# Optimization experiments

Measured on AMD Instinct MI355X. Metric: run time of the kernel, lower is better.

The kernel has to match this reference:

```python
import jax, jax.numpy as jnp
import numpy as np

DIM = 1024; DEPTH = 2; HEADS = 8; DH = DIM // HEADS  # 128
BUCKET = 64; NHASH = 4; MULT = 4
B = 2; T = 4096
NBUCKETS = T // BUCKET  # 64
SCALE = DH ** -0.5
SELF_ATTN_VAL = -5e4  # TOKEN_SELF_ATTN_VALUE in reformer-pytorch
EPS = 1e-5


def layer_norm(x, g, b):
    m = jnp.mean(x, -1, keepdims=True)
    v = jnp.var(x, -1, keepdims=True)
    return (x - m) * jax.lax.rsqrt(v + EPS) * g + b


def lsh_attn(xn, Wqk, Wv, Wo, bo, rot):
    # xn: [B,T,DIM] already layer-normed. Shared-QK LSH attention (reformer-pytorch).
    qk = (xn @ Wqk).reshape(B, T, HEADS, DH).transpose(0, 2, 1, 3).reshape(B * HEADS, T, DH)
    v = (xn @ Wv).reshape(B, T, HEADS, DH).transpose(0, 2, 1, 3).reshape(B * HEADS, T, DH)
    bh = B * HEADS
    # --- hashing with random rotations ---
    rotated = jnp.einsum('btf,fhi->bhti', qk, rot)            # [bh,NHASH,T,NBUCKETS//2]
    rotated = jnp.concatenate([rotated, -rotated], -1)        # [bh,NHASH,T,NBUCKETS]
    buckets = jnp.argmax(rotated, -1)                         # [bh,NHASH,T]
    offs = (jnp.arange(NHASH) * NBUCKETS)[:, None]
    buckets = (buckets + offs).reshape(bh, NHASH * T)
    ticker = jnp.arange(NHASH * T)
    bt = buckets * T + (ticker % T)                           # unique keys -> stable-equivalent sort
    sticker = jnp.argsort(bt, axis=-1)                        # [bh, NHASH*T]
    undo = jnp.argsort(sticker, axis=-1)
    st = sticker % T                                          # original positions, bucket-sorted
    sqk = jnp.take_along_axis(qk, st[..., None], axis=1)
    sv = jnp.take_along_axis(v, st[..., None], axis=1)
    nchunks = NHASH * NBUCKETS
    bq_t = st.reshape(bh, nchunks, BUCKET)
    bqk = sqk.reshape(bh, nchunks, BUCKET, DH)
    bv = sv.reshape(bh, nchunks, BUCKET, DH)
    bq = bqk
    bk = bqk / jnp.clip(jnp.linalg.norm(bqk, axis=-1, keepdims=True), 1e-12)
    def look_one_back(a):
        extra = jnp.concatenate([a[:, -1:], a[:, :-1]], axis=1)
        return jnp.concatenate([a, extra], axis=2)
    bk = look_one_back(bk); bv = look_one_back(bv); bkv_t = look_one_back(bq_t)
    dots = jnp.einsum('bcie,bcje->bcij', bq, bk) * SCALE      # [bh,nchunks,BUCKET,2*BUCKET]
    self_mask = bq_t[..., :, None] == bkv_t[..., None, :]     # shared-QK: penalize i==j
    dots = jnp.where(self_mask, SELF_ATTN_VAL, dots)
    lse = jax.nn.logsumexp(dots, axis=-1, keepdims=True)
    p = jnp.exp(dots - lse)
    bo_ = jnp.einsum('bcij,bcje->bcie', p, bv)
    so = bo_.reshape(bh, NHASH * T, DH)
    slog = lse.reshape(bh, NHASH * T)
    o = jnp.take_along_axis(so, undo[..., None], axis=1)
    logits = jnp.take_along_axis(slog, undo, axis=1)
    o = o.reshape(bh, NHASH, T, DH)
    logits = logits.reshape(bh, NHASH, T, 1)
    probs = jnp.exp(logits - jax.nn.logsumexp(logits, axis=1, keepdims=True))
    out = jnp.sum(o * probs, axis=1)                          # combine hash rounds
    out = out.reshape(B, HEADS, T, DH).transpose(0, 2, 1, 3).reshape(B, T, HEADS * DH)
    return out @ Wo + bo


def setup_inputs() -> dict:
    key = jax.random.key(0)
    ks = jax.random.split(key, 16)
    s = 0.02
    d = {
        'x': jax.random.normal(ks[0], (B, T, DIM), jnp.float32),
        'ln1_g': jnp.ones((DEPTH, DIM), jnp.float32),
        'ln1_b': jnp.zeros((DEPTH, DIM), jnp.float32),
        'Wqk': jax.random.normal(ks[1], (DEPTH, DIM, HEADS * DH), jnp.float32) * s,
        'Wv': jax.random.normal(ks[2], (DEPTH, DIM, HEADS * DH), jnp.float32) * s,
        'Wo': jax.random.normal(ks[3], (DEPTH, HEADS * DH, DIM), jnp.float32) * s,
        'bo': jnp.zeros((DEPTH, DIM), jnp.float32),
        'ln2_g': jnp.ones((DEPTH, DIM), jnp.float32),
        'ln2_b': jnp.zeros((DEPTH, DIM), jnp.float32),
        'W1': jax.random.normal(ks[4], (DEPTH, DIM, DIM * MULT), jnp.float32) * s,
        'b1': jnp.zeros((DEPTH, DIM * MULT), jnp.float32),
        'W2': jax.random.normal(ks[5], (DEPTH, DIM * MULT, DIM), jnp.float32) * s,
        'b2': jnp.zeros((DEPTH, DIM), jnp.float32),
        'rotations': jax.random.normal(ks[6], (DEPTH, DH, NHASH, NBUCKETS // 2), jnp.float32),
    }
    return d


def reference(x, ln1_g, ln1_b, Wqk, Wv, Wo, bo, ln2_g, ln2_b, W1, b1, W2, b2, rotations):
    xx = jnp.concatenate([x, x], -1)  # [B,T,2*DIM] reversible pair
    def step(carry, p):
        g1, be1, wqk, wv, wo, bov, g2, be2, w1, bb1, w2, bb2, rot = p
        x1, x2 = jnp.split(carry, 2, axis=-1)
        y1 = x1 + lsh_attn(layer_norm(x2, g1, be1), wqk, wv, wo, bov, rot)
        h = layer_norm(y1, g2, be2)
        ff = jax.nn.gelu(h @ w1 + bb1, approximate=False) @ w2 + bb2
        y2 = x2 + ff
        return jnp.concatenate([y1, y2], -1), None
    params = (ln1_g, ln1_b, Wqk, Wv, Wo, bo, ln2_g, ln2_b, W1, b1, W2, b2, rotations)
    out, _ = jax.lax.scan(step, xx, params)
    y1, y2 = jnp.split(out, 2, axis=-1)
    return y1 + y2
```

## Files before the change

kernel.cpp:

```cpp
#include <hip/hip_runtime.h>
#include <hip/hip_bf16.h>
#include <cmath>

using bf16 = __hip_bfloat16;
typedef __attribute__((ext_vector_type(8))) short short8;
typedef __attribute__((ext_vector_type(4))) float floatx4;

__device__ __forceinline__ float bu2f(ushort u) { return __uint_as_float((unsigned)u << 16); }
__device__ __forceinline__ ushort f2bu(float f) {
  union { bf16 b; ushort u; } cv; cv.b = __float2bfloat16(f); return cv.u;
}
__device__ __forceinline__ void gl_lds16(const ushort* g, ushort* l) {
  __builtin_amdgcn_global_load_lds((const __attribute__((address_space(1))) unsigned*)g,
                                   (__attribute__((address_space(3))) unsigned*)l, 16, 0, 0);
}
__device__ __forceinline__ float fast_gelu(float x) {
  float z = 0.7978845608028654f * (x + 0.044715f * x * x * x);
  z = fmaxf(fminf(z, 10.f), -10.f);
  float e = __expf(2.f * z);
  float t = (e - 1.f) / (e + 1.f);
  return 0.5f * x * (1.f + t);
}

static constexpr int kT   = 4096;
static constexpr int kDim = 1024;
static constexpr float kScale   = 0.08838834764831845f;
static constexpr float kSelfVal = -5.0e4f;

__device__ __forceinline__ int sane_v(float f) { float a = fabsf(f); return (a > 1e-4f && a < 1e4f) ? 1 : 0; }

__global__ __launch_bounds__(256) void k_detect(const unsigned* __restrict__ x, int* __restrict__ flag) {
  __shared__ int cnt;
  int tid = threadIdx.x;
  if (tid == 0) cnt = 0;
  __syncthreads();
  int my = 0;
  const uint4* p = (const uint4*)x;
  for (int q = 0; q < 16; q++) {
    uint4 u = p[tid * 16 + q];
    my += sane_v(__uint_as_float(u.x << 16)) + sane_v(__uint_as_float(u.x & 0xffff0000u));
    my += sane_v(__uint_as_float(u.y << 16)) + sane_v(__uint_as_float(u.y & 0xffff0000u));
    my += sane_v(__uint_as_float(u.z << 16)) + sane_v(__uint_as_float(u.z & 0xffff0000u));
    my += sane_v(__uint_as_float(u.w << 16)) + sane_v(__uint_as_float(u.w & 0xffff0000u));
  }
  atomicAdd(&cnt, my);
  __syncthreads();
  if (tid == 0) flag[0] = (cnt >= 24576) ? 1 : 0;
}

__global__ __launch_bounds__(256) void k_cvt(const int* __restrict__ flag, const void* __restrict__ src,
                                             ushort* __restrict__ dst, int n) {
  int i = blockIdx.x * 256 + threadIdx.x;
  if (i >= n) return;
  dst[i] = (*flag) ? ((const ushort*)src)[i] : f2bu(((const float*)src)[i]);
}

__global__ __launch_bounds__(256) void k_init_any(const int* __restrict__ flag, const void* __restrict__ x,
                                                  float* __restrict__ x1, float* __restrict__ x2) {
  int i = blockIdx.x * 1024 + threadIdx.x * 4;
  float4 f;
  if (*flag) {
    ushort4 u = *(const ushort4*)((const ushort*)x + i);
    f.x = bu2f(u.x); f.y = bu2f(u.y); f.z = bu2f(u.z); f.w = bu2f(u.w);
  } else {
    f = *(const float4*)((const float*)x + i);
  }
  *(float4*)(x1 + i) = f;
  *(float4*)(x2 + i) = f;
}

__global__ __launch_bounds__(256) void k_final_any(const int* __restrict__ flag, const float* __restrict__ x1,
                                                   const float* __restrict__ x2, void* __restrict__ out) {
  int i = blockIdx.x * 1024 + threadIdx.x * 4;
  float4 a = *(const float4*)(x1 + i);
  float4 b = *(const float4*)(x2 + i);
  float4 s; s.x = a.x + b.x; s.y = a.y + b.y; s.z = a.z + b.z; s.w = a.w + b.w;
  if (*flag) {
    ushort4 u; u.x = f2bu(s.x); u.y = f2bu(s.y); u.z = f2bu(s.z); u.w = f2bu(s.w);
    *(ushort4*)((ushort*)out + i) = u;
  } else {
    *(float4*)((float*)out + i) = s;
  }
}

__global__ __launch_bounds__(256) void k_ln(const float* __restrict__ x, const ushort* __restrict__ g,
                                            const ushort* __restrict__ be, ushort* __restrict__ out) {
  __shared__ float ws[4], ws2[4];
  int row = blockIdx.x, tid = threadIdx.x;
  const float* xr = x + (size_t)row * kDim + tid * 4;
  float4 v = *(const float4*)xr;
  float s  = v.x + v.y + v.z + v.w;
  float s2 = v.x*v.x + v.y*v.y + v.z*v.z + v.w*v.w;
  #pragma unroll
  for (int off = 32; off; off >>= 1) { s += __shfl_down(s, off); s2 += __shfl_down(s2, off); }
  int wave = tid >> 6, lane = tid & 63;
  if (lane == 0) { ws[wave] = s; ws2[wave] = s2; }
  __syncthreads();
  s  = ws[0] + ws[1] + ws[2] + ws[3];
  s2 = ws2[0] + ws2[1] + ws2[2] + ws2[3];
  float mean = s * (1.f/1024.f);
  float var  = fmaxf(s2 * (1.f/1024.f) - mean*mean, 0.f);
  float rstd = rsqrtf(var + 1e-5f);
  int cb = tid * 4;
  ushort* o = out + (size_t)row * kDim + cb;
  o[0] = f2bu((v.x - mean) * rstd * bu2f(g[cb+0]) + bu2f(be[cb+0]));
  o[1] = f2bu((v.y - mean) * rstd * bu2f(g[cb+1]) + bu2f(be[cb+1]));
  o[2] = f2bu((v.z - mean) * rstd * bu2f(g[cb+2]) + bu2f(be[cb+2]));
  o[3] = f2bu((v.w - mean) * rstd * bu2f(g[cb+3]) + bu2f(be[cb+3]));
}

__global__ __launch_bounds__(256) void k_transpose2(const int* __restrict__ flag, const void* __restrict__ src_bf,
                                                    const void* __restrict__ src_f, ushort* __restrict__ out,
                                                    int K, int N) {
  __shared__ ushort tile[32][33];
  int isbf = *flag;
  int nb = blockIdx.x * 32, kb = blockIdx.y * 32;
  int tx = threadIdx.x & 31, ty = threadIdx.x >> 5;
  for (int r = ty; r < 32; r += 8) {
    size_t idx = (size_t)(kb + r) * N + nb + tx;
    tile[r][tx] = isbf ? ((const ushort*)src_bf)[idx] : f2bu(((const float*)src_f)[idx]);
  }
  __syncthreads();
  for (int r = ty; r < 32; r += 8) out[(size_t)(nb + r) * K + kb + tx] = tile[tx][r];
}

__global__ __launch_bounds__(256) void k_rot_t(const ushort* __restrict__ rot, ushort* __restrict__ rotT) {
  int tid = threadIdx.x;
  for (int idx = tid; idx < 16384; idx += 256) {
    int n = idx >> 7, k = idx & 127;
    rotT[idx] = rot[k * 128 + n];
  }
}

template <int MW>
__global__ __launch_bounds__(512, 2) void k_gemm2(const ushort* __restrict__ A, const ushort* __restrict__ Bt,
                                                  const ushort* __restrict__ bias, float* __restrict__ Cf,
                                                  ushort* __restrict__ Cb, ushort* __restrict__ Cb2,
                                                  int M, int N, int K, int mode) {
  constexpr int BM  = MW * 32;
  constexpr int LA  = MW / 4;
  constexpr int AHI = (MW == 8) ? 4 : 2;
  __shared__ alignas(16) ushort SAu[4 * BM * 32];
  __shared__ alignas(16) ushort SBu[4 * 256 * 32];

  const int tid  = threadIdx.x;
  const int lane = tid & 63, wave = tid >> 6;
  const int lr = lane & 15, g = lane >> 4;
  const int wm = wave >> 2, wn = wave & 3;

  const int nbx = gridDim.x;
  const int nwg = nbx * gridDim.y;
  const int bid = blockIdx.y * nbx + blockIdx.x;
  const int swz = (bid & 7) * (nwg >> 3) + (bid >> 3);
  const int m0 = (swz / nbx) * BM;
  const int n0 = (swz % nbx) * 256;

  const int NT = K >> 5;

  const ushort* srcA[LA];
  #pragma unroll
  for (int j = 0; j < LA; j++) {
    int chunk = wave * (64 * LA) + j * 64 + lane;
    int row = chunk >> 2, c = chunk & 3;
    int cs = c ^ ((row >> 1) & 3);
    srcA[j] = A + (size_t)(m0 + row) * K + cs * 8;
  }
  const ushort* srcB[2];
  #pragma unroll
  for (int j = 0; j < 2; j++) {
    int chunk = wave * 128 + j * 64 + lane;
    int row = chunk >> 2, c = chunk & 3;
    int cs = c ^ ((row >> 1) & 3);
    srcB[j] = Bt + (size_t)(n0 + row) * K + cs * 8;
  }

  int offA[MW], offB[4];
  #pragma unroll
  for (int mi = 0; mi < MW; mi++) {
    int row = wm * (MW * 16) + mi * 16 + lr;
    offA[mi] = row * 32 + ((g ^ ((row >> 1) & 3)) * 8);
  }
  #pragma unroll
  for (int ni = 0; ni < 4; ni++) {
    int row = wn * 64 + ni * 16 + lr;
    offB[ni] = row * 32 + ((g ^ ((row >> 1) & 3)) * 8);
  }

  floatx4 acc[MW][4];
  #pragma unroll
  for (int mi = 0; mi < MW; mi++)
    #pragma unroll
    for (int ni = 0; ni < 4; ni++) acc[mi][ni] = (floatx4){0.f, 0.f, 0.f, 0.f};

  #pragma unroll
  for (int p = 0; p < 3; p++) {
    #pragma unroll
    for (int j = 0; j < LA; j++) gl_lds16(srcA[j] + p * 32, SAu + p * (BM * 32) + (wave * (64 * LA) + j * 64) * 8);
    #pragma unroll
    for (int j = 0; j < 2; j++)  gl_lds16(srcB[j] + p * 32, SBu + p * (256 * 32) + (wave * 128 + j * 64) * 8);
  }
  if constexpr (MW == 8) asm volatile("s_waitcnt vmcnt(8)" ::: "memory");
  else                   asm volatile("s_waitcnt vmcnt(6)" ::: "memory");
  __builtin_amdgcn_s_barrier();
  asm volatile("" ::: "memory");

  for (int kt = 0; kt < NT; kt++) {
    const ushort* sa = SAu + (kt & 3) * (BM * 32);
    const ushort* sb = SBu + (kt & 3) * (256 * 32);
    const bool pf = (kt + 3 < NT);
    const int kp = (kt + 3) * 32, pb = (kt + 3) & 3;

    short8 aA[AHI], bb[4];
    #pragma unroll
    for (int i = 0; i < AHI; i++) aA[i] = *(const short8*)&sa[offA[i]];
    #pragma unroll
    for (int ni = 0; ni < 4; ni++) bb[ni] = *(const short8*)&sb[offB[ni]];
    if (pf) {
      if constexpr (MW == 8) {
        gl_lds16(srcA[0] + kp, SAu + pb * (BM * 32) + (wave * 128 + 0) * 8);
        gl_lds16(srcA[1] + kp, SAu + pb * (BM * 32) + (wave * 128 + 64) * 8);
      } else {
        gl_lds16(srcA[0] + kp, SAu + pb * (BM * 32) + (wave * 64) * 8);
        gl_lds16(srcB[0] + kp, SBu + pb * (256 * 32) + (wave * 128 + 0) * 8);
      }
    }
    __builtin_amdgcn_s_barrier();
    asm volatile("" ::: "memory");
    __builtin_amdgcn_s_setprio(1);
    #pragma unroll
    for (int mi = 0; mi < AHI; mi++)
      #pragma unroll
      for (int ni = 0; ni < 4; ni++)
        acc[mi][ni] = __builtin_amdgcn_mfma_f32_16x16x32_bf16(aA[mi], bb[ni], acc[mi][ni], 0, 0, 0);
    __builtin_amdgcn_s_setprio(0);
    __builtin_amdgcn_sched_barrier(0);
    __builtin_amdgcn_s_barrier();
    asm volatile("" ::: "memory");

    short8 aB[MW - AHI];
    #pragma unroll
    for (int i = 0; i < MW - AHI; i++) aB[i] = *(const short8*)&sa[offA[AHI + i]];
    if (pf) {
      if constexpr (MW == 8) {
        gl_lds16(srcB[0] + kp, SBu + pb * (256 * 32) + (wave * 128 + 0) * 8);
        gl_lds16(srcB[1] + kp, SBu + pb * (256 * 32) + (wave * 128 + 64) * 8);
      } else {
        gl_lds16(srcB[1] + kp, SBu + pb * (256 * 32) + (wave * 128 + 64) * 8);
      }
    }
    if (kt + 3 < NT) {
      if constexpr (MW == 8) asm volatile("s_waitcnt vmcnt(8)" ::: "memory");
      else                   asm volatile("s_waitcnt vmcnt(6)" ::: "memory");
    } else if (kt + 2 < NT) {
      if constexpr (MW == 8) asm volatile("s_waitcnt vmcnt(4)" ::: "memory");
      else                   asm volatile("s_waitcnt vmcnt(3)" ::: "memory");
    } else if (kt + 1 < NT) {
      asm volatile("s_waitcnt vmcnt(0)" ::: "memory");
    }
    __builtin_amdgcn_s_barrier();
    asm volatile("" ::: "memory");
    __builtin_amdgcn_s_setprio(1);
    #pragma unroll
    for (int mi = 0; mi < MW - AHI; mi++)
      #pragma unroll
      for (int ni = 0; ni < 4; ni++)
        acc[AHI + mi][ni] = __builtin_amdgcn_mfma_f32_16x16x32_bf16(aB[mi], bb[ni], acc[AHI + mi][ni], 0, 0, 0);
    __builtin_amdgcn_s_setprio(0);
    __builtin_amdgcn_sched_barrier(0);
    __builtin_amdgcn_s_barrier();
    asm volatile("" ::: "memory");
  }

  const int hi4 = (lane >> 4) * 4;

  if (mode == 1) {
    #pragma unroll
    for (int mi = 0; mi < MW; mi++) {
      #pragma unroll
      for (int ni = 0; ni < 4; ni++) {
        int col = n0 + wn * 64 + ni * 16 + lr;
        float bv = bu2f(bias[col]);
        #pragma unroll
        for (int q = 0; q < 4; q++) {
          int r2 = m0 + wm * (MW * 16) + mi * 16 + hi4 + q;
          Cf[(size_t)r2 * N + col] += acc[mi][ni][q] + bv;
        }
      }
    }
  } else {
    ushort* reg0 = (MW == 8) ? SAu : SBu;
    ushort* reg1 = SBu;
    #pragma unroll
    for (int mi = 0; mi < MW; mi++) {
      #pragma unroll
      for (int ni = 0; ni < 4; ni++) {
        int colw = wn * 64 + ni * 16 + lr;
        float bv = (mode == 2) ? bu2f(bias[n0 + colw]) : 0.f;
        #pragma unroll
        for (int q = 0; q < 4; q++) {
          int grow = wm * (MW * 16) + mi * 16 + hi4 + q;
          ushort* reg = (grow < 128) ? reg0 : reg1;
          int rl = grow & 127;
          float val = acc[mi][ni][q];
          ushort h = (mode == 2) ? f2bu(fast_gelu(val + bv)) : f2bu(val);
          reg[rl * 256 + (((colw >> 3) ^ (rl & 7)) * 8) + (colw & 7)] = h;
        }
      }
    }
    __syncthreads();
    {
      const int j = tid & 31;
      const int rsub = tid >> 5;
      #pragma unroll
      for (int p = 0; p < BM / 16; p++) {
        int row = p * 16 + rsub;
        const ushort* reg = (row < 128) ? reg0 : reg1;
        int rl = row & 127;
        short8 v = *(const short8*)&reg[rl * 256 + ((j ^ (rl & 7)) * 8)];
        *(short8*)&Cb[(size_t)(m0 + row) * N + n0 + j * 8] = v;
      }
    }
    if (mode == 5) {
      __syncthreads();
      #pragma unroll
      for (int mi = 0; mi < MW; mi++) {
        #pragma unroll
        for (int ni = 0; ni < 4; ni++) {
          int colw = wn * 64 + ni * 16 + lr;
          #pragma unroll
          for (int q = 0; q < 4; q++) {
            int grow = wm * (MW * 16) + mi * 16 + hi4 + q;
            ushort* reg = (grow < 128) ? reg0 : reg1;
            int rl = grow & 127;
            float val = acc[mi][ni][q];
            ushort h = f2bu(val);
            reg[rl * 256 + (((colw >> 3) ^ (rl & 7)) * 8) + (colw & 7)] = f2bu(val - bu2f(h));
          }
        }
      }
      __syncthreads();
      const int j = tid & 31;
      const int rsub = tid >> 5;
      #pragma unroll
      for (int p = 0; p < BM / 16; p++) {
        int row = p * 16 + rsub;
        const ushort* reg = (row < 128) ? reg0 : reg1;
        int rl = row & 127;
        short8 v = *(const short8*)&reg[rl * 256 + ((j ^ (rl & 7)) * 8)];
        *(short8*)&Cb2[(size_t)(m0 + row) * N + n0 + j * 8] = v;
      }
    }
  }
  (void)M;
}

__global__ __launch_bounds__(256) void k_bucket_mfma(const ushort* __restrict__ qkh, const ushort* __restrict__ qkl,
                                                     const ushort* __restrict__ rotT, int* __restrict__ bkt) {
  __shared__ alignas(16) ushort Bs[128*128];
  __shared__ alignas(16) ushort Ah[64*128];
  __shared__ alignas(16) ushort Al[64*128];
  const int tid = threadIdx.x;
  const int lane = tid & 63, wave = tid >> 6;
  const int lr = lane & 15, lk = (lane >> 4) * 8;
  const int tt = blockIdx.x * 64;
  const int bh = blockIdx.y;
  const int b = bh >> 3, hh = bh & 7;

  {
    int r = tid >> 2, c0 = (tid & 3) * 32;
    size_t base = ((size_t)(b * kT + tt + r)) * kDim + hh * 128 + c0;
    const uint4* sh = (const uint4*)(qkh + base);
    const uint4* sl = (const uint4*)(qkl + base);
    uint4* dh = (uint4*)&Ah[r * 128 + c0];
    uint4* dl = (uint4*)&Al[r * 128 + c0];
    #pragma unroll
    for (int i = 0; i < 4; i++) { dh[i] = sh[i]; dl[i] = sl[i]; }
  }
  {
    const uint4* src = (const uint4*)rotT;
    uint4* dst = (uint4*)Bs;
    for (int i = tid; i < 2048; i += 256) dst[i] = src[i];
  }
  __syncthreads();

  floatx4 acc[4][2];
  #pragma unroll
  for (int mi = 0; mi < 4; mi++) { acc[mi][0] = (floatx4){0,0,0,0}; acc[mi][1] = (floatx4){0,0,0,0}; }
  #pragma unroll
  for (int ks = 0; ks < 4; ks++) {
    short8 a[4], bb[2];
    #pragma unroll
    for (int ni = 0; ni < 2; ni++) bb[ni] = *(const short8*)&Bs[(wave*32 + ni*16 + lr)*128 + ks*32 + lk];
    #pragma unroll
    for (int mi = 0; mi < 4; mi++) a[mi] = *(const short8*)&Ah[(mi*16 + lr)*128 + ks*32 + lk];
    #pragma unroll
    for (int mi = 0; mi < 4; mi++)
      #pragma unroll
      for (int ni = 0; ni < 2; ni++)
        acc[mi][ni] = __builtin_amdgcn_mfma_f32_16x16x32_bf16(a[mi], bb[ni], acc[mi][ni], 0, 0, 0);
  }
  #pragma unroll
  for (int ks = 0; ks < 4; ks++) {
    short8 a[4], bb[2];
    #pragma unroll
    for (int ni = 0; ni < 2; ni++) bb[ni] = *(const short8*)&Bs[(wave*32 + ni*16 + lr)*128 + ks*32 + lk];
    #pragma unroll
    for (int mi = 0; mi < 4; mi++) a[mi] = *(const short8*)&Al[(mi*16 + lr)*128 + ks*32 + lk];
    #pragma unroll
    for (int mi = 0; mi < 4; mi++)
      #pragma unroll
      for (int ni = 0; ni < 2; ni++)
        acc[mi][ni] = __builtin_amdgcn_mfma_f32_16x16x32_bf16(a[mi], bb[ni], acc[mi][ni], 0, 0, 0);
  }

  #pragma unroll
  for (int mi = 0; mi < 4; mi++) {
    #pragma unroll
    for (int q = 0; q < 4; q++) {
      float v0 = acc[mi][0][q];
      float v1 = acc[mi][1][q];
      float best = v0; int bidx = lr;
      if (v1  > best) { best = v1;  bidx = 16 + lr; }
      if (-v0 > best) { best = -v0; bidx = 32 + lr; }
      if (-v1 > best) { best = -v1; bidx = 48 + lr; }
      #pragma unroll
      for (int m = 1; m <= 8; m <<= 1) {
        float ov = __shfl_xor(best, m);
        int   oi = __shfl_xor(bidx, m);
        if (ov > best || (ov == best && oi < bidx)) { best = ov; bidx = oi; }
      }
      if (lr == 0) {
        int row = mi*16 + ((lane >> 4) & 3)*4 + q;
        bkt[(bh*4 + wave)*4096 + tt + row] = bidx;
      }
    }
  }
}

__global__ __launch_bounds__(256) void k_sort(const int* __restrict__ bkt, int* __restrict__ st) {
  __shared__ unsigned char  hist[64*256];
  __shared__ unsigned short offs[64*256];
  __shared__ int base[64];
  int tid = threadIdx.x, grp = blockIdx.x;
  const int* bk = bkt + grp * 4096;
  for (int i = tid; i < 64*256; i += 256) hist[i] = 0;
  __syncthreads();
  int myb[16];
  #pragma unroll
  for (int j = 0; j < 16; j++) {
    myb[j] = bk[tid*16 + j];
    hist[myb[j]*256 + tid] += 1;
  }
  __syncthreads();
  if (tid < 64) {
    int run = 0;
    for (int t = 0; t < 256; t++) { offs[tid*256 + t] = (unsigned short)run; run += hist[tid*256 + t]; }
    base[tid] = run;
  }
  __syncthreads();
  if (tid == 0) {
    int run = 0;
    for (int b2 = 0; b2 < 64; b2++) { int c = base[b2]; base[b2] = run; run += c; }
  }
  __syncthreads();
  #pragma unroll
  for (int j = 0; j < 16; j++) {
    int b2 = myb[j];
    int r = 0;
    for (int jj = 0; jj < j; jj++) r += (myb[jj] == b2) ? 1 : 0;
    st[grp*4096 + base[b2] + (int)offs[b2*256 + tid] + r] = tid*16 + j;
  }
}

__global__ __launch_bounds__(256) void k_attn(const ushort* __restrict__ qkh, const ushort* __restrict__ vbuf,
                                              const int* __restrict__ st, ushort* __restrict__ o_r,
                                              float* __restrict__ lse_r) {
  __shared__ alignas(16) ushort KV[128*136];
  __shared__ alignas(16) ushort Ps[64*136];
  __shared__ float rnorm[128];
  __shared__ int   kposs[128];
  __shared__ float red1[64*4];
  __shared__ float red2[64*4];
  __shared__ float lrow[64];

  const int tid = threadIdx.x;
  const int bid = blockIdx.x;
  const int bh = bid >> 8;
  const int c  = bid & 255;
  const int h  = c >> 6;
  const int cprev = (c + 255) & 255;
  const int b  = bh >> 3, hh = bh & 7;
  const int lane = tid & 63, wave = tid >> 6;
  const int lr = lane & 15, lk = (lane >> 4) * 8;

  {
    int j = tid >> 1, half = tid & 1;
    int slot = (j < 64) ? (c*64 + j) : (cprev*64 + (j - 64));
    int pos = st[bh*16384 + slot];
    if (half == 0) kposs[j] = pos;
    const ushort* src = qkh + ((size_t)(b * kT + pos)) * kDim + hh*128 + half*64;
    float ss = 0.f;
    #pragma unroll
    for (int i2 = 0; i2 < 64; i2 += 8) {
      uint4 u = *(const uint4*)(src + i2);
      *(uint4*)&KV[j*136 + half*64 + i2] = u;
      float f0 = bu2f((ushort)(u.x & 0xffffu)), f1 = bu2f((ushort)(u.x >> 16));
      float f2 = bu2f((ushort)(u.y & 0xffffu)), f3 = bu2f((ushort)(u.y >> 16));
      float f4 = bu2f((ushort)(u.z & 0xffffu)), f5 = bu2f((ushort)(u.z >> 16));
      float f6 = bu2f((ushort)(u.w & 0xffffu)), f7 = bu2f((ushort)(u.w >> 16));
      ss += f0*f0 + f1*f1 + f2*f2 + f3*f3 + f4*f4 + f5*f5 + f6*f6 + f7*f7;
    }
    ss += __shfl_xor(ss, 1);
    if (half == 0) rnorm[j] = 1.f / fmaxf(sqrtf(ss), 1e-12f);
  }
  __syncthreads();

  {
    floatx4 acc[4][2];
    #pragma unroll
    for (int mi = 0; mi < 4; mi++) { acc[mi][0] = (floatx4){0,0,0,0}; acc[mi][1] = (floatx4){0,0,0,0}; }
    #pragma unroll
    for (int ks = 0; ks < 4; ks++) {
      short8 a[4], bb[2];
      #pragma unroll
      for (int mi = 0; mi < 4; mi++) a[mi]  = *(const short8*)&KV[(mi*16 + lr)*136 + ks*32 + lk];
      #pragma unroll
      for (int ni = 0; ni < 2; ni++) bb[ni] = *(const short8*)&KV[(wave*32 + ni*16 + lr)*136 + ks*32 + lk];
      #pragma unroll
      for (int mi = 0; mi < 4; mi++)
        #pragma unroll
        for (int ni = 0; ni < 2; ni++)
          acc[mi][ni] = __builtin_amdgcn_mfma_f32_16x16x32_bf16(a[mi], bb[ni], acc[mi][ni], 0, 0, 0);
    }
    #pragma unroll
    for (int mi = 0; mi < 4; mi++) {
      #pragma unroll
      for (int ni = 0; ni < 2; ni++) {
        int col = wave*32 + ni*16 + lr;
        float rn = rnorm[col] * kScale;
        int cpos = kposs[col];
        #pragma unroll
        for (int q = 0; q < 4; q++) {
          int row = mi*16 + (lane >> 4)*4 + q;
          float val = acc[mi][ni][q] * rn;
          if (cpos == kposs[row]) val = kSelfVal;
          Ps[row*136 + col] = f2bu(val);
        }
      }
    }
  }
  __syncthreads();

  {
    int j = tid >> 1, half = tid & 1;
    int pos = kposs[j];
    const ushort* src = vbuf + ((size_t)(b * kT + pos)) * kDim + hh*128 + half*64;
    #pragma unroll
    for (int i2 = 0; i2 < 64; i2 += 8) {
      uint4 u = *(const uint4*)(src + i2);
      int d0 = half*64 + i2;
      KV[(d0+0)*136 + j] = (ushort)(u.x & 0xffffu); KV[(d0+1)*136 + j] = (ushort)(u.x >> 16);
      KV[(d0+2)*136 + j] = (ushort)(u.y & 0xffffu); KV[(d0+3)*136 + j] = (ushort)(u.y >> 16);
      KV[(d0+4)*136 + j] = (ushort)(u.z & 0xffffu); KV[(d0+5)*136 + j] = (ushort)(u.z >> 16);
      KV[(d0+6)*136 + j] = (ushort)(u.w & 0xffffu); KV[(d0+7)*136 + j] = (ushort)(u.w >> 16);
    }
  }

  {
    int i = tid >> 2, part = tid & 3;
    const int jb = part * 32;
    float m = -1e30f;
    for (int j2 = 0; j2 < 32; j2++) m = fmaxf(m, bu2f(Ps[i*136 + jb + j2]));
    red1[i*4 + part] = m;
    __syncthreads();
    m = fmaxf(fmaxf(red1[i*4+0], red1[i*4+1]), fmaxf(red1[i*4+2], red1[i*4+3]));
    float ssum = 0.f;
    for (int j2 = 0; j2 < 32; j2++) {
      float arg = fmaxf(fminf(bu2f(Ps[i*136 + jb + j2]) - m, 0.f), -80.f);
      float p = __expf(arg);
      ssum += p;
      Ps[i*136 + jb + j2] = f2bu(p);
    }
    red2[i*4 + part] = ssum;
    __syncthreads();
    if (part == 0) {
      float l = fmaxf(red2[i*4+0] + red2[i*4+1] + red2[i*4+2] + red2[i*4+3], 1e-20f);
      lrow[i] = 1.f / l;
      lse_r[(size_t)(bh*4 + h)*4096 + kposs[i]] = m + __logf(l);
    }
  }
  __syncthreads();

  {
    floatx4 acc[4][2];
    #pragma unroll
    for (int mi = 0; mi < 4; mi++) { acc[mi][0] = (floatx4){0,0,0,0}; acc[mi][1] = (floatx4){0,0,0,0}; }
    #pragma unroll
    for (int ks = 0; ks < 4; ks++) {
      short8 a[4], bb[2];
      #pragma unroll
      for (int mi = 0; mi < 4; mi++) a[mi]  = *(const short8*)&Ps[(mi*16 + lr)*136 + ks*32 + lk];
      #pragma unroll
      for (int ni = 0; ni < 2; ni++) bb[ni] = *(const short8*)&KV[(wave*32 + ni*16 + lr)*136 + ks*32 + lk];
      #pragma unroll
      for (int mi = 0; mi < 4; mi++)
        #pragma unroll
        for (int ni = 0; ni < 2; ni++)
          acc[mi][ni] = __builtin_amdgcn_mfma_f32_16x16x32_bf16(a[mi], bb[ni], acc[mi][ni], 0, 0, 0);
    }
    #pragma unroll
    for (int mi = 0; mi < 4; mi++) {
      #pragma unroll
      for (int ni = 0; ni < 2; ni++) {
        int d = wave*32 + ni*16 + lr;
        #pragma unroll
        for (int q = 0; q < 4; q++) {
          int row = mi*16 + (lane >> 4)*4 + q;
          float o = acc[mi][ni][q] * lrow[row];
          o_r[((size_t)(bh*4 + h)*4096 + kposs[row])*128 + d] = f2bu(o);
        }
      }
    }
  }
}

__global__ __launch_bounds__(256) void k_combine(const ushort* __restrict__ o_r, const float* __restrict__ lse_r,
                                                 ushort* __restrict__ attnbf) {
  int rid = blockIdx.x * 2 + (threadIdx.x >> 7);
  int d = threadIdx.x & 127;
  int bh = rid >> 12, t = rid & 4095;
  int b = bh >> 3, hh = bh & 7;
  size_t base = (size_t)bh * 16384 + t;
  float l0 = lse_r[base], l1 = lse_r[base + 4096], l2 = lse_r[base + 8192], l3 = lse_r[base + 12288];
  float M = fmaxf(fmaxf(l0, l1), fmaxf(l2, l3));
  float e0 = __expf(fmaxf(fminf(l0 - M, 0.f), -80.f));
  float e1 = __expf(fmaxf(fminf(l1 - M, 0.f), -80.f));
  float e2 = __expf(fmaxf(fminf(l2 - M, 0.f), -80.f));
  float e3 = __expf(fmaxf(fminf(l3 - M, 0.f), -80.f));
  float inv = 1.f / (e0 + e1 + e2 + e3);
  float o = e0 * bu2f(o_r[(base         )*128 + d]) + e1 * bu2f(o_r[(base +  4096)*128 + d])
          + e2 * bu2f(o_r[(base +  8192)*128 + d]) + e3 * bu2f(o_r[(base + 12288)*128 + d]);
  attnbf[((size_t)b * kT + t) * kDim + hh*128 + d] = f2bu(o * inv);
}

extern "C" void kernel_launch(void* const* d_in, const int* in_sizes, int n_in,
                              void* d_out, int out_size, void* d_ws, size_t ws_size,
                              hipStream_t stream) {
  (void)in_sizes; (void)n_in; (void)out_size; (void)ws_size;
  const void* x     = d_in[0];
  const void* ln1_g = d_in[1];
  const void* ln1_b = d_in[2];
  const void* Wqk   = d_in[3];
  const void* Wv    = d_in[4];
  const void* Wo    = d_in[5];
  const void* bo    = d_in[6];
  const void* ln2_g = d_in[7];
  const void* ln2_b = d_in[8];
  const void* W1    = d_in[9];
  const void* b1    = d_in[10];
  const void* W2    = d_in[11];
  const void* b2    = d_in[12];
  const void* rot   = d_in[13];

  char* w = (char*)d_ws;
  int*    flag = (int*)w;    w += 256;
  ushort* prm  = (ushort*)w; w += 131072;
  float* x1  = (float*)w;  w += 33554432;
  float* x2  = (float*)w;  w += 33554432;
  ushort* qkh = (ushort*)w; w += 16777216;
  ushort* qkl = (ushort*)w; w += 16777216;
  ushort* vbb = (ushort*)w; w += 16777216;
  ushort* xbf = (ushort*)w; w += 16777216;
  ushort* orb = (ushort*)w; w += 67108864;
  float* lse = (float*)w;  w += 1048576;
  int*   bkt = (int*)w;    w += 1048576;
  int*   stb = (int*)w;    w += 1048576;
  ushort* wtA = (ushort*)w; w += 2097152;
  ushort* wtB = (ushort*)w; w += 2097152;
  ushort* wtC = (ushort*)w; w += 2097152;
  ushort* wt1 = (ushort*)w; w += 8388608;
  ushort* wt2 = (ushort*)w; w += 8388608;
  ushort* rtT = (ushort*)w; w += 32768;

  ushort* pLN1G = prm + 0;     ushort* pLN1B = prm + 2048;
  ushort* pBO   = prm + 4096;  ushort* pLN2G = prm + 6144;
  ushort* pLN2B = prm + 8192;  ushort* pB1   = prm + 10240;
  ushort* pB2   = prm + 18432; ushort* pROT  = prm + 20480;

  k_detect<<<1, 256, 0, stream>>>((const unsigned*)x, flag);
  k_cvt<<<8,   256, 0, stream>>>(flag, ln1_g, pLN1G, 2048);
  k_cvt<<<8,   256, 0, stream>>>(flag, ln1_b, pLN1B, 2048);
  k_cvt<<<8,   256, 0, stream>>>(flag, bo,    pBO,   2048);
  k_cvt<<<8,   256, 0, stream>>>(flag, ln2_g, pLN2G, 2048);
  k_cvt<<<8,   256, 0, stream>>>(flag, ln2_b, pLN2B, 2048);
  k_cvt<<<32,  256, 0, stream>>>(flag, b1,    pB1,   8192);
  k_cvt<<<8,   256, 0, stream>>>(flag, b2,    pB2,   2048);
  k_cvt<<<128, 256, 0, stream>>>(flag, rot,   pROT,  32768);
  k_init_any<<<8192, 256, 0, stream>>>(flag, x, x1, x2);

  for (int d = 0; d < 2; d++) {
    k_transpose2<<<dim3(32, 32),  256, 0, stream>>>(flag,
        (const char*)Wqk + (size_t)d*1048576*2, (const char*)Wqk + (size_t)d*1048576*4, wtA, 1024, 1024);
    k_transpose2<<<dim3(32, 32),  256, 0, stream>>>(flag,
        (const char*)Wv  + (size_t)d*1048576*2, (const char*)Wv  + (size_t)d*1048576*4, wtB, 1024, 1024);
    k_transpose2<<<dim3(32, 32),  256, 0, stream>>>(flag,
        (const char*)Wo  + (size_t)d*1048576*2, (const char*)Wo  + (size_t)d*1048576*4, wtC, 1024, 1024);
    k_transpose2<<<dim3(128, 32), 256, 0, stream>>>(flag,
        (const char*)W1  + (size_t)d*4194304*2, (const char*)W1  + (size_t)d*4194304*4, wt1, 1024, 4096);
    k_transpose2<<<dim3(32, 128), 256, 0, stream>>>(flag,
        (const char*)W2  + (size_t)d*4194304*2, (const char*)W2  + (size_t)d*4194304*4, wt2, 4096, 1024);
    k_rot_t<<<1, 256, 0, stream>>>(pROT + (size_t)d * 16384, rtT);

    k_ln<<<8192, 256, 0, stream>>>(x2, pLN1G + d*1024, pLN1B + d*1024, xbf);
    k_gemm2<4><<<dim3(4, 64), 512, 0, stream>>>(xbf, wtA, nullptr, nullptr, qkh, qkl, 8192, 1024, 1024, 5);
    k_gemm2<4><<<dim3(4, 64), 512, 0, stream>>>(xbf, wtB, nullptr, nullptr, vbb, nullptr, 8192, 1024, 1024, 3);
    k_bucket_mfma<<<dim3(64, 16), 256, 0, stream>>>(qkh, qkl, rtT, bkt);
    k_sort<<<64, 256, 0, stream>>>(bkt, stb);
    k_attn<<<4096, 256, 0, stream>>>(qkh, vbb, stb, orb, lse);
    k_combine<<<32768, 256, 0, stream>>>(orb, lse, xbf);
    k_gemm2<4><<<dim3(4, 64), 512, 0, stream>>>(xbf, wtC, pBO + d*1024, x1, nullptr, nullptr, 8192, 1024, 1024, 1);
    k_ln<<<8192, 256, 0, stream>>>(x1, pLN2G + d*1024, pLN2B + d*1024, xbf);
    k_gemm2<8><<<dim3(16, 32), 512, 0, stream>>>(xbf, wt1, pB1 + d*4096, nullptr, orb, nullptr, 8192, 4096, 1024, 2);
    k_gemm2<4><<<dim3(4, 64), 512, 0, stream>>>(orb, wt2, pB2 + d*1024, x2, nullptr, nullptr, 8192, 1024, 4096, 1);
  }
  k_final_any<<<8192, 256, 0, stream>>>(flag, x1, x2, d_out);
}
```

Baseline: 1.182 ms.

## Add dedicated 256x256 K64 double-buffered GEMM for FFN up-projection with GELU

Adds k_gemm3, a 256x256-tile bf16 MFMA GEMM that stages K=64 slices into two LDS buffers. It interleaves global-to-LDS loads with the MFMA phases under explicit barriers and vmcnt waits, and fuses bias plus GELU into a swizzled LDS-staged epilogue. It also applies a block-ID swizzle for L2 locality and replaces the generic k_gemm2<8> launch for the W1 projection. Existing k_gemm2 barriers now use sched_barrier instead of an asm memory clobber. The hand-tuned wait counts and fixed tile assumptions add correctness and portability risk.

```diff
diff --git a/kernel.cpp b/kernel.cpp
--- a/kernel.cpp
+++ b/kernel.cpp
@@ -225,7 +225,7 @@
       }
     }
     __builtin_amdgcn_s_barrier();
-    asm volatile("" ::: "memory");
+    __builtin_amdgcn_sched_barrier(0);
     __builtin_amdgcn_s_setprio(1);
     #pragma unroll
     for (int mi = 0; mi < AHI; mi++)
@@ -258,7 +258,7 @@
       asm volatile("s_waitcnt vmcnt(0)" ::: "memory");
     }
     __builtin_amdgcn_s_barrier();
-    asm volatile("" ::: "memory");
+    __builtin_amdgcn_sched_barrier(0);
     __builtin_amdgcn_s_setprio(1);
     #pragma unroll
     for (int mi = 0; mi < MW - AHI; mi++)
@@ -352,6 +352,169 @@
     }
   }
   (void)M;
+}
+
+__global__ __launch_bounds__(512, 2) void k_gemm3(const ushort* __restrict__ A, const ushort* __restrict__ Bt,
+                                                  const ushort* __restrict__ bias, ushort* __restrict__ Cb,
+                                                  int M, int N, int K) {
+  __shared__ alignas(16) ushort SA[2 * 256 * 64];
+  __shared__ alignas(16) ushort SB[2 * 256 * 64];
+  const int tid  = threadIdx.x;
+  const int lane = tid & 63, wave = tid >> 6;
+  const int lr = lane & 15, g = lane >> 4;
+  const int wm = wave >> 2, wn = wave & 3;
+
+  const int nbx = gridDim.x;
+  const int nwg = nbx * gridDim.y;
+  const int bid = blockIdx.y * nbx + blockIdx.x;
+  const int swz = (bid & 7) * (nwg >> 3) + (bid >> 3);
+  const int m0 = (swz / nbx) * 256;
+  const int n0 = (swz % nbx) * 256;
+  const int NT = K >> 6;
+  const int NI = NT >> 1;
+
+  const int chAr = (wave * 64 + lane) >> 3;
+  const int chAs = (wave * 64 + lane) & 7;
+  const int swA  = (chAs ^ (chAr & 7)) * 8;
+  const ushort* sAq[2][2];
+  #pragma unroll
+  for (int q = 0; q < 2; q++)
+    #pragma unroll
+    for (int j = 0; j < 2; j++)
+      sAq[q][j] = A + (size_t)(m0 + q * 64 + j * 128 + chAr) * K + swA;
+  const int chBr = lane >> 3;
+  const int swB  = ((lane & 7) ^ chBr) * 8;
+  const ushort* sBh[2][2];
+  #pragma unroll
+  for (int h = 0; h < 2; h++)
+    #pragma unroll
+    for (int j = 0; j < 2; j++)
+      sBh[h][j] = Bt + (size_t)(n0 + h * 128 + wave * 16 + j * 8 + chBr) * K + swB;
+
+  int rA[8], rB[4], cK[2];
+  #pragma unroll
+  for (int mi = 0; mi < 8; mi++) rA[mi] = (wm * 128 + mi * 16 + lr) * 64;
+  #pragma unroll
+  for (int ni = 0; ni < 4; ni++) rB[ni] = (wn * 64 + ni * 16 + lr) * 64;
+  cK[0] = ((0 * 4 + g) ^ (lr & 7)) * 8;
+  cK[1] = ((1 * 4 + g) ^ (lr & 7)) * 8;
+
+  floatx4 acc[8][4];
+  #pragma unroll
+  for (int mi = 0; mi < 8; mi++)
+    #pragma unroll
+    for (int ni = 0; ni < 4; ni++) acc[mi][ni] = (floatx4){0.f, 0.f, 0.f, 0.f};
+
+#define G3_STG_A(d, q, kt) { int ko = ((kt) < NT ? (kt) : 0) << 6; \
+    gl_lds16(sAq[q][0] + ko, SA + (d) * 16384 + ((q) * 64 + wave * 8) * 64); \
+    gl_lds16(sAq[q][1] + ko, SA + (d) * 16384 + (128 + (q) * 64 + wave * 8) * 64); }
+#define G3_STG_B(d, h, kt) { int ko = ((kt) < NT ? (kt) : 0) << 6; \
+    gl_lds16(sBh[h][0] + ko, SB + (d) * 16384 + ((h) * 128 + wave * 16) * 64); \
+    gl_lds16(sBh[h][1] + ko, SB + (d) * 16384 + ((h) * 128 + wave * 16 + 8) * 64); }
+#define G3_RD_A(dst, d, kk, mb) { _Pragma("unroll") \
+    for (int _m = 0; _m < 4; _m++) dst[_m] = *(const short8*)&SA[(d) * 16384 + rA[(mb) + _m] + cK[kk]]; }
+#define G3_RD_B(dst, d, kk) { _Pragma("unroll") \
+    for (int _n = 0; _n < 4; _n++) dst[_n] = *(const short8*)&SB[(d) * 16384 + rB[_n] + cK[kk]]; }
+#define G3_MM(mb, af, bf) { \
+    __builtin_amdgcn_s_setprio(1); \
+    _Pragma("unroll") for (int _m = 0; _m < 4; _m++) \
+      _Pragma("unroll") for (int _n = 0; _n < 4; _n++) \
+        acc[(mb) + _m][_n] = __builtin_amdgcn_mfma_f32_16x16x32_bf16(af[_m], bf[_n], acc[(mb) + _m][_n], 0, 0, 0); \
+    __builtin_amdgcn_s_setprio(0); }
+#define G3_BAR()  __builtin_amdgcn_s_barrier()
+#define G3_SB()   __builtin_amdgcn_sched_barrier(0)
+
+  G3_STG_A(0, 0, 0); G3_STG_A(0, 1, 0); G3_STG_B(0, 0, 0); G3_STG_B(0, 1, 0);
+  G3_STG_A(1, 0, 1); G3_STG_B(1, 0, 1);
+  asm volatile("s_waitcnt vmcnt(4)" ::: "memory");
+  G3_BAR();
+  asm volatile("" ::: "memory");
+
+  for (int i = 0; i < NI; i++) {
+    const int kb = 2 * i;
+    short8 aA[4], bb0[4], bb1[4];
+    G3_RD_A(aA, 0, 0, 0); G3_RD_B(bb0, 0, 0); G3_STG_B(1, 1, kb + 1);
+    G3_BAR(); G3_SB();
+    G3_MM(0, aA, bb0);
+    G3_SB(); G3_BAR(); asm volatile("" ::: "memory");
+    G3_RD_A(aA, 0, 1, 0); G3_RD_B(bb1, 0, 1); G3_STG_A(1, 1, kb + 1);
+    G3_BAR(); G3_SB();
+    G3_MM(0, aA, bb1);
+    G3_SB(); G3_BAR(); asm volatile("" ::: "memory");
+    G3_RD_A(aA, 0, 0, 4); G3_STG_A(0, 0, kb + 2);
+    G3_BAR(); G3_SB();
+    G3_MM(4, aA, bb0);
+    G3_SB(); G3_BAR(); asm volatile("" ::: "memory");
+    G3_RD_A(aA, 0, 1, 4); G3_STG_B(0, 0, kb + 2);
+    G3_BAR(); G3_SB();
+    G3_MM(4, aA, bb1);
+    G3_SB();
+    asm volatile("s_waitcnt vmcnt(6)" ::: "memory");
+    G3_BAR(); asm volatile("" ::: "memory");
+    G3_RD_A(aA, 1, 0, 0); G3_RD_B(bb0, 1, 0); G3_STG_B(0, 1, kb + 2);
+    G3_BAR(); G3_SB();
+    G3_MM(0, aA, bb0);
+    G3_SB(); G3_BAR(); asm volatile("" ::: "memory");
+    G3_RD_A(aA, 1, 1, 0); G3_RD_B(bb1, 1, 1); G3_STG_A(0, 1, kb + 2);
+    G3_BAR(); G3_SB();
+    G3_MM(0, aA, bb1);
+    G3_SB();
+    asm volatile("s_waitcnt vmcnt(8)" ::: "memory");
+    G3_BAR(); asm volatile("" ::: "memory");
+    G3_RD_A(aA, 1, 0, 4); G3_STG_A(1, 0, kb + 3);
+    G3_BAR(); G3_SB();
+    G3_MM(4, aA, bb0);
+    G3_SB(); G3_BAR(); asm volatile("" ::: "memory");
+    G3_RD_A(aA, 1, 1, 4); G3_STG_B(1, 0, kb + 3);
+    G3_BAR(); G3_SB();
+    G3_MM(4, aA, bb1);
+    G3_SB();
+    asm volatile("s_waitcnt vmcnt(4)" ::: "memory");
+    G3_BAR(); asm volatile("" ::: "memory");
+  }
+
+  asm volatile("s_waitcnt vmcnt(0)" ::: "memory");
+  __syncthreads();
+
+  const int hi4 = (lane >> 4) * 4;
+  ushort* reg0 = SA;
+  ushort* reg1 = SB;
+  #pragma unroll
+  for (int mi = 0; mi < 8; mi++) {
+    #pragma unroll
+    for (int ni = 0; ni < 4; ni++) {
+      int colw = wn * 64 + ni * 16 + lr;
+      float bv = bu2f(bias[n0 + colw]);
+      #pragma unroll
+      for (int q = 0; q < 4; q++) {
+        int grow = wm * 128 + mi * 16 + hi4 + q;
+        ushort* reg = (grow < 128) ? reg0 : reg1;
+        int rl = grow & 127;
+        reg[rl * 256 + (((colw >> 3) ^ (rl & 7)) * 8) + (colw & 7)] = f2bu(fast_gelu(acc[mi][ni][q] + bv));
+      }
+    }
+  }
+  __syncthreads();
+  {
+    const int j = tid & 31;
+    const int rsub = tid >> 5;
+    #pragma unroll
+    for (int p = 0; p < 16; p++) {
+      int row = p * 16 + rsub;
+      const ushort* reg = (row < 128) ? reg0 : reg1;
+      int rl = row & 127;
+      short8 v = *(const short8*)&reg[rl * 256 + ((j ^ (rl & 7)) * 8)];
+      *(short8*)&Cb[(size_t)(m0 + row) * N + n0 + j * 8] = v;
+    }
+  }
+  (void)M;
+#undef G3_STG_A
+#undef G3_STG_B
+#undef G3_RD_A
+#undef G3_RD_B
+#undef G3_MM
+#undef G3_BAR
+#undef G3_SB
 }
 
 __global__ __launch_bounds__(256) void k_bucket_mfma(const ushort* __restrict__ qkh, const ushort* __restrict__ qkl,
@@ -720,7 +883,7 @@
     k_combine<<<32768, 256, 0, stream>>>(orb, lse, xbf);
     k_gemm2<4><<<dim3(4, 64), 512, 0, stream>>>(xbf, wtC, pBO + d*1024, x1, nullptr, nullptr, 8192, 1024, 1024, 1);
     k_ln<<<8192, 256, 0, stream>>>(x1, pLN2G + d*1024, pLN2B + d*1024, xbf);
-    k_gemm2<8><<<dim3(16, 32), 512, 0, stream>>>(xbf, wt1, pB1 + d*4096, nullptr, orb, nullptr, 8192, 4096, 1024, 2);
+    k_gemm3<<<dim3(16, 32), 512, 0, stream>>>(xbf, wt1, pB1 + d*4096, orb, 8192, 4096, 1024);
     k_gemm2<4><<<dim3(4, 64), 512, 0, stream>>>(orb, wt2, pB2 + d*1024, x2, nullptr, nullptr, 8192, 1024, 4096, 1);
   }
   k_final_any<<<8192, 256, 0, stream>>>(flag, x1, x2, d_out);
```

Result: no change. 1.170 ms (-1.0%).

## Restructure GEMM main loop into single-barrier, full-tile prefetch pipeline

Applied to the files above, without the earlier changes.

Replaces the two-phase ping-pong main loop (split MFMA halves, split prefetch, four barriers per k-step) with a simpler loop. Each iteration loads every A and B fragment from LDS, issues the whole next-stage prefetch, runs all MFMAs, then waits and takes one barrier. The prefetch depth drops to 2 stages for the MW=8 variant and stays at 3 for MW=4. Out-of-range prefetches are clamped to k=0 rather than skipped, and a final vmcnt(0) plus sync drains them. This cuts barrier overhead but loses the interleaving between loads and MFMAs, which raises register pressure and risks exposing memory latency.

```diff
diff --git a/kernel.cpp b/kernel.cpp
--- a/kernel.cpp
+++ b/kernel.cpp
@@ -133,13 +133,13 @@
 }
 
 template <int MW>
-__global__ __launch_bounds__(512, 2) void k_gemm2(const ushort* __restrict__ A, const ushort* __restrict__ Bt,
+__global__ __launch_bounds__(512, 2) void k_gemm5(const ushort* __restrict__ A, const ushort* __restrict__ Bt,
                                                   const ushort* __restrict__ bias, float* __restrict__ Cf,
                                                   ushort* __restrict__ Cb, ushort* __restrict__ Cb2,
                                                   int M, int N, int K, int mode) {
-  constexpr int BM  = MW * 32;
-  constexpr int LA  = MW / 4;
-  constexpr int AHI = (MW == 8) ? 4 : 2;
+  constexpr int BM = MW * 32;
+  constexpr int LA = MW / 4;
+  constexpr int PF = (MW == 8) ? 2 : 3;
   __shared__ alignas(16) ushort SAu[4 * BM * 32];
   __shared__ alignas(16) ushort SBu[4 * 256 * 32];
 
@@ -193,13 +193,13 @@
     for (int ni = 0; ni < 4; ni++) acc[mi][ni] = (floatx4){0.f, 0.f, 0.f, 0.f};
 
   #pragma unroll
-  for (int p = 0; p < 3; p++) {
+  for (int p = 0; p < PF; p++) {
     #pragma unroll
     for (int j = 0; j < LA; j++) gl_lds16(srcA[j] + p * 32, SAu + p * (BM * 32) + (wave * (64 * LA) + j * 64) * 8);
     #pragma unroll
     for (int j = 0; j < 2; j++)  gl_lds16(srcB[j] + p * 32, SBu + p * (256 * 32) + (wave * 128 + j * 64) * 8);
   }
-  if constexpr (MW == 8) asm volatile("s_waitcnt vmcnt(8)" ::: "memory");
+  if constexpr (MW == 8) asm volatile("s_waitcnt vmcnt(4)" ::: "memory");
   else                   asm volatile("s_waitcnt vmcnt(6)" ::: "memory");
   __builtin_amdgcn_s_barrier();
   asm volatile("" ::: "memory");
@@ -207,69 +207,36 @@
   for (int kt = 0; kt < NT; kt++) {
     const ushort* sa = SAu + (kt & 3) * (BM * 32);
     const ushort* sb = SBu + (kt & 3) * (256 * 32);
-    const bool pf = (kt + 3 < NT);
-    const int kp = (kt + 3) * 32, pb = (kt + 3) & 3;
-
-    short8 aA[AHI], bb[4];
-    #pragma unroll
-    for (int i = 0; i < AHI; i++) aA[i] = *(const short8*)&sa[offA[i]];
-    #pragma unroll
-    for (int ni = 0; ni < 4; ni++) bb[ni] = *(const short8*)&sb[offB[ni]];
-    if (pf) {
-      if constexpr (MW == 8) {
-        gl_lds16(srcA[0] + kp, SAu + pb * (BM * 32) + (wave * 128 + 0) * 8);
-        gl_lds16(srcA[1] + kp, SAu + pb * (BM * 32) + (wave * 128 + 64) * 8);
-      } else {
-        gl_lds16(srcA[0] + kp, SAu + pb * (BM * 32) + (wave * 64) * 8);
-        gl_lds16(srcB[0] + kp, SBu + pb * (256 * 32) + (wave * 128 + 0) * 8);
-      }
-    }
+    const int kp = ((kt + PF < NT) ? (kt + PF) : 0) * 32;
+    const int pb = (kt + PF) & 3;
+
+    short8 a[MW], b[4];
+    #pragma unroll
+    for (int mi = 0; mi < MW; mi++) a[mi] = *(const short8*)&sa[offA[mi]];
+    #pragma unroll
+    for (int ni = 0; ni < 4; ni++)  b[ni] = *(const short8*)&sb[offB[ni]];
+
+    #pragma unroll
+    for (int j = 0; j < LA; j++) gl_lds16(srcA[j] + kp, SAu + pb * (BM * 32) + (wave * (64 * LA) + j * 64) * 8);
+    #pragma unroll
+    for (int j = 0; j < 2; j++)  gl_lds16(srcB[j] + kp, SBu + pb * (256 * 32) + (wave * 128 + j * 64) * 8);
+
+    __builtin_amdgcn_s_setprio(1);
+    #pragma unroll
+    for (int mi = 0; mi < MW; mi++)
+      #pragma unroll
+      for (int ni = 0; ni < 4; ni++)
+        acc[mi][ni] = __builtin_amdgcn_mfma_f32_16x16x32_bf16(a[mi], b[ni], acc[mi][ni], 0, 0, 0);
+    __builtin_amdgcn_s_setprio(0);
+
+    if constexpr (MW == 8) asm volatile("s_waitcnt vmcnt(4)" ::: "memory");
+    else                   asm volatile("s_waitcnt vmcnt(6)" ::: "memory");
     __builtin_amdgcn_s_barrier();
     asm volatile("" ::: "memory");
-    __builtin_amdgcn_s_setprio(1);
-    #pragma unroll
-    for (int mi = 0; mi < AHI; mi++)
-      #pragma unroll
-      for (int ni = 0; ni < 4; ni++)
-        acc[mi][ni] = __builtin_amdgcn_mfma_f32_16x16x32_bf16(aA[mi], bb[ni], acc[mi][ni], 0, 0, 0);
-    __builtin_amdgcn_s_setprio(0);
-    __builtin_amdgcn_sched_barrier(0);
-    __builtin_amdgcn_s_barrier();
-    asm volatile("" ::: "memory");
-
-    short8 aB[MW - AHI];
-    #pragma unroll
-    for (int i = 0; i < MW - AHI; i++) aB[i] = *(const short8*)&sa[offA[AHI + i]];
-    if (pf) {
-      if constexpr (MW == 8) {
-        gl_lds16(srcB[0] + kp, SBu + pb * (256 * 32) + (wave * 128 + 0) * 8);
-        gl_lds16(srcB[1] + kp, SBu + pb * (256 * 32) + (wave * 128 + 64) * 8);
-      } else {
-        gl_lds16(srcB[1] + kp, SBu + pb * (256 * 32) + (wave * 128 + 64) * 8);
-      }
-    }
-    if (kt + 3 < NT) {
-      if constexpr (MW == 8) asm volatile("s_waitcnt vmcnt(8)" ::: "memory");
-      else                   asm volatile("s_waitcnt vmcnt(6)" ::: "memory");
-    } else if (kt + 2 < NT) {
-      if constexpr (MW == 8) asm volatile("s_waitcnt vmcnt(4)" ::: "memory");
-      else                   asm volatile("s_waitcnt vmcnt(3)" ::: "memory");
-    } else if (kt + 1 < NT) {
-      asm volatile("s_waitcnt vmcnt(0)" ::: "memory");
-    }
-    __builtin_amdgcn_s_barrier();
-    asm volatile("" ::: "memory");
-    __builtin_amdgcn_s_setprio(1);
-    #pragma unroll
-    for (int mi = 0; mi < MW - AHI; mi++)
-      #pragma unroll
-      for (int ni = 0; ni < 4; ni++)
-        acc[AHI + mi][ni] = __builtin_amdgcn_mfma_f32_16x16x32_bf16(aB[mi], bb[ni], acc[AHI + mi][ni], 0, 0, 0);
-    __builtin_amdgcn_s_setprio(0);
-    __builtin_amdgcn_sched_barrier(0);
-    __builtin_amdgcn_s_barrier();
-    asm volatile("" ::: "memory");
-  }
+  }
+
+  asm volatile("s_waitcnt vmcnt(0)" ::: "memory");
+  __syncthreads();
 
   const int hi4 = (lane >> 4) * 4;
 
@@ -712,16 +679,16 @@
     k_rot_t<<<1, 256, 0, stream>>>(pROT + (size_t)d * 16384, rtT);
 
     k_ln<<<8192, 256, 0, stream>>>(x2, pLN1G + d*1024, pLN1B + d*1024, xbf);
-    k_gemm2<4><<<dim3(4, 64), 512, 0, stream>>>(xbf, wtA, nullptr, nullptr, qkh, qkl, 8192, 1024, 1024, 5);
-    k_gemm2<4><<<dim3(4, 64), 512, 0, stream>>>(xbf, wtB, nullptr, nullptr, vbb, nullptr, 8192, 1024, 1024, 3);
+    k_gemm5<4><<<dim3(4, 64), 512, 0, stream>>>(xbf, wtA, nullptr, nullptr, qkh, qkl, 8192, 1024, 1024, 5);
+    k_gemm5<4><<<dim3(4, 64), 512, 0, stream>>>(xbf, wtB, nullptr, nullptr, vbb, nullptr, 8192, 1024, 1024, 3);
     k_bucket_mfma<<<dim3(64, 16), 256, 0, stream>>>(qkh, qkl, rtT, bkt);
     k_sort<<<64, 256, 0, stream>>>(bkt, stb);
     k_attn<<<4096, 256, 0, stream>>>(qkh, vbb, stb, orb, lse);
     k_combine<<<32768, 256, 0, stream>>>(orb, lse, xbf);
-    k_gemm2<4><<<dim3(4, 64), 512, 0, stream>>>(xbf, wtC, pBO + d*1024, x1, nullptr, nullptr, 8192, 1024, 1024, 1);
+    k_gemm5<4><<<dim3(4, 64), 512, 0, stream>>>(xbf, wtC, pBO + d*1024, x1, nullptr, nullptr, 8192, 1024, 1024, 1);
     k_ln<<<8192, 256, 0, stream>>>(x1, pLN2G + d*1024, pLN2B + d*1024, xbf);
-    k_gemm2<8><<<dim3(16, 32), 512, 0, stream>>>(xbf, wt1, pB1 + d*4096, nullptr, orb, nullptr, 8192, 4096, 1024, 2);
-    k_gemm2<4><<<dim3(4, 64), 512, 0, stream>>>(orb, wt2, pB2 + d*1024, x2, nullptr, nullptr, 8192, 1024, 4096, 1);
+    k_gemm5<8><<<dim3(16, 32), 512, 0, stream>>>(xbf, wt1, pB1 + d*4096, nullptr, orb, nullptr, 8192, 4096, 1024, 2);
+    k_gemm5<4><<<dim3(4, 64), 512, 0, stream>>>(orb, wt2, pB2 + d*1024, x2, nullptr, nullptr, 8192, 1024, 4096, 1);
   }
   k_final_any<<<8192, 256, 0, stream>>>(flag, x1, x2, d_out);
 }
```

Measured after the change: 1.108 ms. 1.07x faster.
